# Kernel tuning notes

Hardware: AMD Instinct MI355X
Metric: run time of the kernel (lower is better)

Reference implementation:

```python
import jax, jax.numpy as jnp
import numpy as np

NB, T, NS, NC = 1024, 128, 12, 4
N = NS + NC  # stacked state+control dim


def setup_inputs() -> dict:
    key = jax.random.key(0)
    ks = jax.random.split(key, 7)
    x_init = jax.random.normal(ks[0], (NB, NS), jnp.float32)
    current_x = jax.random.normal(ks[1], (NB, T, NS), jnp.float32)
    current_u = jax.random.normal(ks[2], (NB, T, NC), jnp.float32)
    # symmetric positive-definite cost Hessian per (batch, t)
    G = 0.1 * jax.random.normal(ks[3], (NB, T, N, N), jnp.float32)
    Q = 0.5 * (G + jnp.swapaxes(G, -1, -2)) + jnp.eye(N, dtype=jnp.float32)
    p = jax.random.normal(ks[4], (NB, T, N), jnp.float32)
    # stable per-step dynamics linearizations
    A = 0.95 * jnp.eye(NS, dtype=jnp.float32) + 0.02 * jax.random.normal(ks[5], (NB, T, NS, NS), jnp.float32)
    Bmat = 0.1 * jax.random.normal(ks[6], (NB, T, NS, NC), jnp.float32)
    time = jnp.arange(T, dtype=jnp.int32)
    return {"x_init": x_init, "current_x": current_x, "current_u": current_u,
            "Q": Q, "p": p, "A": A, "Bmat": Bmat, "time": time}


def _lqr_backward(Q, p, A, Bmat):
    # time-major for scan: (T, NB, ...)
    Qs = jnp.moveaxis(Q, 1, 0)
    ps = jnp.moveaxis(p, 1, 0)
    As = jnp.moveaxis(A, 1, 0)
    Bs = jnp.moveaxis(Bmat, 1, 0)
    nb = Q.shape[0]
    V0 = jnp.zeros((nb, NS, NS), Q.dtype)  # V=0 reproduces the t==T-1 branch
    v0 = jnp.zeros((nb, NS), Q.dtype)

    def step(carry, inp):
        V, v = carry
        Qt0, pt, At, Bt = inp
        F = jnp.concatenate([At, Bt], axis=-1)          # (nb, ns, n)
        FT = jnp.swapaxes(F, -1, -2)                    # (nb, n, ns)
        Qt = Qt0 + FT @ V @ F                           # (nb, n, n)
        qt = pt + jnp.einsum('bsn,bs->bn', F, v)        # F^T v
        Qxx, Qxu = Qt[..., :NS, :NS], Qt[..., :NS, NS:]
        Qux, Quu = Qt[..., NS:, :NS], Qt[..., NS:, NS:]
        qx, qu = qt[..., :NS], qt[..., NS:]
        Quu_inv = jnp.linalg.pinv(Quu)                  # (nb, nc, nc)
        Kt = -(Quu_inv @ Qux)                           # (nb, nc, ns)
        kt = -jnp.einsum('bij,bj->bi', Quu_inv, qu)     # (nb, nc)
        KtT = jnp.swapaxes(Kt, -1, -2)
        Vn = Qxx + Qxu @ Kt + KtT @ Qux + KtT @ Quu @ Kt
        vn = (qx + jnp.einsum('bij,bj->bi', Qxu, kt)
              + jnp.einsum('bij,bj->bi', KtT, qu)
              + jnp.einsum('bij,bj->bi', KtT @ Quu, kt))
        return (Vn, vn), (Kt, kt)

    _, (K, k) = jax.lax.scan(step, (V0, v0), (Qs, ps, As, Bs), reverse=True)
    return jnp.moveaxis(K, 0, 1), jnp.moveaxis(k, 0, 1)


def _lqr_forward(x_init, current_u, Q, p, A, Bmat, K, k):
    Ks = jnp.moveaxis(K, 1, 0)
    ks_ = jnp.moveaxis(k, 1, 0)
    As = jnp.moveaxis(A, 1, 0)
    Bs = jnp.moveaxis(Bmat, 1, 0)
    cus = jnp.moveaxis(current_u, 1, 0)
    Qs = jnp.moveaxis(Q, 1, 0)
    ps = jnp.moveaxis(p, 1, 0)
    nb = x_init.shape[0]
    cost0 = jnp.zeros((nb,), x_init.dtype)

    def step(carry, inp):
        xt, cost = carry
        Kt, kt, At, Bt, cut, Qt, pt = inp
        # NOTE: original module never updates delta_x (stays zero), so delta_u == k_t
        ut = cut + kt
        xut = jnp.concatenate([xt, ut], axis=-1)        # (nb, n)
        xnext = jnp.einsum('bij,bj->bi', At, xt) + jnp.einsum('bij,bj->bi', Bt, ut)
        cost = cost + 0.5 * jnp.einsum('bi,bij,bj->b', xut, Qt, xut) + jnp.sum(xut * pt, axis=-1)
        return (xnext, cost), (xt, ut)

    (_, cost), (xs, us) = jax.lax.scan(step, (x_init, cost0), (Ks, ks_, As, Bs, cus, Qs, ps))
    # xs holds x_0..x_{T-1}, matching return of x[..., 0:-1, :]
    return jnp.moveaxis(xs, 0, 1), jnp.moveaxis(us, 0, 1), cost


def reference(x_init, current_x, current_u, Q, p, A, Bmat, time):
    K, k = _lqr_backward(Q, p, A, Bmat)
    return _lqr_forward(x_init, current_u, Q, p, A, Bmat, K, k)
```

## Files before the change

### kernel.cpp

```cpp
#include <hip/hip_runtime.h>


#define NBQ 1024
#define TT  128

__device__ __forceinline__ float dotf4(float4 a, float4 b) {
  return a.x*b.x + a.y*b.y + a.z*b.z + a.w*b.w;
}
__device__ __forceinline__ float dpp_qx1(float x) {
  return __int_as_float(__builtin_amdgcn_mov_dpp(__float_as_int(x), 0xB1, 0xF, 0xF, true));
}
__device__ __forceinline__ float dpp_qx2(float x) {
  return __int_as_float(__builtin_amdgcn_mov_dpp(__float_as_int(x), 0x4E, 0xF, 0xF, true));
}

#define BW_BODY(T_, QV, PV, CV, APrev, BPrev, ASelf, BSelf)                    \
{                                                                              \
  const int  t_   = (T_);                                                      \
  const long bt_  = b*TT + t_;                                                 \
  const int  tL_  = (t_ >= 4) ? (t_ - 4) : 0;                                  \
  const long btL_ = b*TT + tL_;                                                \
  float4 qN_ = *(const float4*)(Qg  + btL_*256 + 4*l);                         \
  float4 aN_ = *(const float4*)(Ag  + btL_*144 + aoff);                        \
  float4 bN_ = *(const float4*)(Bg  + btL_*48  + boff);                        \
  float  pN_ = pg[btL_*16 + j];                                                \
  float  cN_ = cug[btL_*4 + q4];                                               \
  float* FTc_ = (t_ & 1) ? FT1 : FT0;                                          \
  float* FTn_ = (t_ & 1) ? FT0 : FT1;                                          \
                         \
  if (l < 36) { FTn_[fta[0]]=APrev.x; FTn_[fta[1]]=APrev.y;                    \
                FTn_[fta[2]]=APrev.z; FTn_[fta[3]]=APrev.w; }                  \
  else if (l < 48) { const int kk_=l-36;                                       \
    FTn_[144+kk_]=BPrev.x; FTn_[156+kk_]=BPrev.y;                              \
    FTn_[168+kk_]=BPrev.z; FTn_[180+kk_]=BPrev.w; }                            \
                                                    \
  const float4* fj4_ = (const float4*)(FTc_ + j*12);                           \
  float4 f0_=fj4_[0], f1_=fj4_[1], f2_=fj4_[2];                                \
  const float4* gi4_ = (const float4*)(FTc_ + i4*12);                          \
  float4 g0_=gi4_[0], g1_=gi4_[1], g2_=gi4_[2];                                \
  const float4* vv4_ = (const float4*)vvS;                                     \
  float4 w0_=vv4_[0], w1_=vv4_[1], w2_=vv4_[2];                                \
  const float4* vr0_ = (const float4*)(Vs + (3*r+0)*12);                       \
  const float4* vr1_ = (const float4*)(Vs + (3*r+1)*12);                       \
  const float4* vr2_ = (const float4*)(Vs + (3*r+2)*12);                       \
  float4 va0_=vr0_[0], va1_=vr0_[1], va2_=vr0_[2];                             \
  float4 vb0_=vr1_[0], vb1_=vr1_[1], vb2_=vr1_[2];                             \
  float4 vc0_=vr2_[0], vc1_=vr2_[1], vc2_=vr2_[2];                             \
  float m0_ = dotf4(va0_,f0_) + dotf4(va1_,f1_) + dotf4(va2_,f2_);             \
  float m1_ = dotf4(vb0_,f0_) + dotf4(vb1_,f1_) + dotf4(vb2_,f2_);             \
  float m2_ = dotf4(vc0_,f0_) + dotf4(vc1_,f1_) + dotf4(vc2_,f2_);             \
  msh[(3*r+0)*16 + j] = m0_;                                                   \
  msh[(3*r+1)*16 + j] = m1_;                                                   \
  msh[(3*r+2)*16 + j] = m2_;                                                   \
  float qtv_ = PV + dotf4(w0_,f0_) + dotf4(w1_,f1_) + dotf4(w2_,f2_);          \
  float gk_[12] = {g0_.x,g0_.y,g0_.z,g0_.w, g1_.x,g1_.y,g1_.z,g1_.w,           \
                   g2_.x,g2_.y,g2_.z,g2_.w};                                   \
  float4 qt4_ = QV;                                                            \
  _Pragma("unroll")                                                            \
  for (int k2_ = 0; k2_ < 12; ++k2_) {                                         \
    float4 mk_ = *(const float4*)(msh + k2_*16 + c0);                          \
    qt4_.x += gk_[k2_]*mk_.x; qt4_.y += gk_[k2_]*mk_.y;                        \
    qt4_.z += gk_[k2_]*mk_.z; qt4_.w += gk_[k2_]*mk_.w;                        \
  }                                                                            \
  if (l >= 48)            *(float4*)(UxS + (i4-12)*16 + c0) = qt4_;            \
  if (q4 == 3 && i4 < 12) *(float4*)(XuS + i4*4) = qt4_;                       \
  if (l >= 12 && l < 16)  quS[l-12] = qtv_;                                    \
  float mm_[16];                                                               \
  _Pragma("unroll")                                                            \
  for (int c_ = 0; c_ < 4; ++c_) {                                             \
    float4 qq_ = *(const float4*)(UxS + c_*16 + 12);                           \
    mm_[c_*4+0]=qq_.x; mm_[c_*4+1]=qq_.y; mm_[c_*4+2]=qq_.z; mm_[c_*4+3]=qq_.w;\
  }                                                                            \
  float4 quv_ = *(const float4*)quS;                                           \
  float4 ux0_ = *(const float4*)(UxS + 0*16 + c0);                             \
  float4 ux1_ = *(const float4*)(UxS + 1*16 + c0);                             \
  float4 ux2_ = *(const float4*)(UxS + 2*16 + c0);                             \
  float4 ux3_ = *(const float4*)(UxS + 3*16 + c0);                             \
  float4 xr_ = *(const float4*)(XuS + min(i4,11)*4);                           \
  float4 xj_ = *(const float4*)(XuS + min(j,11)*4);                            \
                                       \
  float rdp_ = 1.0f/(mm_[0]*mm_[5] - mm_[1]*mm_[1]);                           \
  float pi00_ = mm_[5]*rdp_, pi01_ = -mm_[1]*rdp_, pi11_ = mm_[0]*rdp_;        \
  float w00_ = pi00_*mm_[2] + pi01_*mm_[6];                                    \
  float w01_ = pi00_*mm_[3] + pi01_*mm_[7];                                    \
  float w10_ = pi01_*mm_[2] + pi11_*mm_[6];                                    \
  float w11_ = pi01_*mm_[3] + pi11_*mm_[7];                                    \
  float t00_ = mm_[10] - (mm_[2]*w00_ + mm_[6]*w10_);                          \
  float t01_ = mm_[11] - (mm_[2]*w01_ + mm_[6]*w11_);                          \
  float t11_ = mm_[15] - (mm_[3]*w01_ + mm_[7]*w11_);                          \
  float rdt_ = 1.0f/(t00_*t11_ - t01_*t01_);                                   \
  float ti00_ = t11_*rdt_, ti01_ = -t01_*rdt_, ti11_ = t00_*rdt_;              \
  float u00_ = -(w00_*ti00_ + w01_*ti01_);                                     \
  float u01_ = -(w00_*ti01_ + w01_*ti11_);                                     \
  float u10_ = -(w10_*ti00_ + w11_*ti01_);                                     \
  float u11_ = -(w10_*ti01_ + w11_*ti11_);                                     \
  float i00_ = pi00_ - (u00_*w00_ + u01_*w01_);                                \
  float i01_ = pi01_ - (u00_*w10_ + u01_*w11_);                                \
  float i11_ = pi11_ - (u10_*w10_ + u11_*w11_);                                \
  float inv_[16] = { i00_, i01_, u00_, u01_,                                   \
                     i01_, i11_, u10_, u11_,                                   \
                     u00_, u10_, ti00_, ti01_,                                 \
                     u01_, u11_, ti01_, ti11_ };                               \
  float kt0_ = -(inv_[0] *quv_.x + inv_[1] *quv_.y + inv_[2] *quv_.z + inv_[3] *quv_.w); \
  float kt1_ = -(inv_[4] *quv_.x + inv_[5] *quv_.y + inv_[6] *quv_.z + inv_[7] *quv_.w); \
  float kt2_ = -(inv_[8] *quv_.x + inv_[9] *quv_.y + inv_[10]*quv_.z + inv_[11]*quv_.w); \
  float kt3_ = -(inv_[12]*quv_.x + inv_[13]*quv_.y + inv_[14]*quv_.z + inv_[15]*quv_.w); \
  float4 kc_[4];                                                               \
  _Pragma("unroll")                                                            \
  for (int c_ = 0; c_ < 4; ++c_) {                                             \
    kc_[c_].x = -(inv_[c_*4+0]*ux0_.x + inv_[c_*4+1]*ux1_.x + inv_[c_*4+2]*ux2_.x + inv_[c_*4+3]*ux3_.x); \
    kc_[c_].y = -(inv_[c_*4+0]*ux0_.y + inv_[c_*4+1]*ux1_.y + inv_[c_*4+2]*ux2_.y + inv_[c_*4+3]*ux3_.y); \
    kc_[c_].z = -(inv_[c_*4+0]*ux0_.z + inv_[c_*4+1]*ux1_.z + inv_[c_*4+2]*ux2_.z + inv_[c_*4+3]*ux3_.z); \
    kc_[c_].w = -(inv_[c_*4+0]*ux0_.w + inv_[c_*4+1]*ux1_.w + inv_[c_*4+2]*ux2_.w + inv_[c_*4+3]*ux3_.w); \
  }                                                                            \
  if (i4 < 12) {                                                               \
    float4 vn4_;                                                               \
    vn4_.x = qt4_.x + xr_.x*kc_[0].x + xr_.y*kc_[1].x + xr_.z*kc_[2].x + xr_.w*kc_[3].x; \
    vn4_.y = qt4_.y + xr_.x*kc_[0].y + xr_.y*kc_[1].y + xr_.z*kc_[2].y + xr_.w*kc_[3].y; \
    vn4_.z = qt4_.z + xr_.x*kc_[0].z + xr_.y*kc_[1].z + xr_.z*kc_[2].z + xr_.w*kc_[3].z; \
    vn4_.w = qt4_.w + xr_.x*kc_[0].w + xr_.y*kc_[1].w + xr_.z*kc_[2].w + xr_.w*kc_[3].w; \
    if (q4 < 3) *(float4*)(Vs + i4*12 + c0) = vn4_;                            \
  }                                                                            \
  if (l < 12)                                                                  \
    vvS[l] = qtv_ + xj_.x*kt0_ + xj_.y*kt1_ + xj_.z*kt2_ + xj_.w*kt3_;         \
  float uv_ = CV + ((q4==0)?kt0_:(q4==1)?kt1_:(q4==2)?kt2_:kt3_);              \
  if (l < 4) { us_out[bt_*4 + l] = uv_; uL[t_*4 + l] = uv_; }                  \
  QV = qN_; ASelf = aN_; BSelf = bN_; PV = pN_; CV = cN_;                      \
}

__global__ __launch_bounds__(64, 1) void lqr_fused(
    const float* __restrict__ Qg, const float* __restrict__ pg,
    const float* __restrict__ Ag, const float* __restrict__ Bg,
    const float* __restrict__ cug, const float* __restrict__ xinit,
    float* __restrict__ out)
{
  __shared__ __align__(16) float lds[1376];
  float* FT0 = lds;
  float* FT1 = lds + 192;
  float* Vs  = lds + 384;
  float* vvS = lds + 528;
  float* msh = lds + 544;
  float* UxS = lds + 736;
  float* XuS = lds + 800;
  float* quS = lds + 848;
  float* uL  = lds + 864;

  const int l  = threadIdx.x;
  const int j  = l & 15;
  const int r  = l >> 4;
  const int i4 = l >> 2;
  const int q4 = l & 3;
  const int c0 = q4 << 2;
  const long b = blockIdx.x;

  float* xs_out = out;
  float* us_out = out + (long)NBQ*TT*12;
  float* c_out  = out + (long)NBQ*TT*12 + (long)NBQ*TT*4;

  if (i4 < 12 && q4 < 3) *(float4*)(Vs + i4*12 + c0) = make_float4(0.f,0.f,0.f,0.f);
  if (l < 12) vvS[l] = 0.f;

  const int aoff = 4*min(l,35);
  const int boff = 4*min(max(l-36,0),11);
  int fta[4];
  #pragma unroll
  for (int e=0;e<4;++e){ int flat=4*l+e; int k=(flat*171)>>11; int n=flat-12*k; fta[e]=n*12+k; }

  const long base = b*TT;
  float4 q3v,a3v,b3v, q2v,a2v,b2v, q1v,a1v,b1v, q0v,a0v,b0v;
  float  p3v,c3v, p2v,c2v, p1v,c1v, p0v,c0vv;
  {
    long bt;
    bt = base+127; q3v=*(const float4*)(Qg+bt*256+4*l); a3v=*(const float4*)(Ag+bt*144+aoff);
                   b3v=*(const float4*)(Bg+bt*48+boff); p3v=pg[bt*16+j]; c3v=cug[bt*4+q4];
    bt = base+126; q2v=*(const float4*)(Qg+bt*256+4*l); a2v=*(const float4*)(Ag+bt*144+aoff);
                   b2v=*(const float4*)(Bg+bt*48+boff); p2v=pg[bt*16+j]; c2v=cug[bt*4+q4];
    bt = base+125; q1v=*(const float4*)(Qg+bt*256+4*l); a1v=*(const float4*)(Ag+bt*144+aoff);
                   b1v=*(const float4*)(Bg+bt*48+boff); p1v=pg[bt*16+j]; c1v=cug[bt*4+q4];
    bt = base+124; q0v=*(const float4*)(Qg+bt*256+4*l); a0v=*(const float4*)(Ag+bt*144+aoff);
                   b0v=*(const float4*)(Bg+bt*48+boff); p0v=pg[bt*16+j]; c0vv=cug[bt*4+q4];
  }
  if (l < 36) {
    FT1[fta[0]]=a3v.x; FT1[fta[1]]=a3v.y; FT1[fta[2]]=a3v.z; FT1[fta[3]]=a3v.w;
  } else if (l < 48) {
    const int kk=l-36;
    FT1[144+kk]=b3v.x; FT1[156+kk]=b3v.y; FT1[168+kk]=b3v.z; FT1[180+kk]=b3v.w;
  }

  #pragma unroll 1
  for (int tb = TT-1; tb >= 3; tb -= 4) {
    BW_BODY(tb,   q3v, p3v, c3v,  a2v, b2v,  a3v, b3v)
    BW_BODY(tb-1, q2v, p2v, c2v,  a1v, b1v,  a2v, b2v)
    BW_BODY(tb-2, q1v, p1v, c1v,  a0v, b0v,  a1v, b1v)
    BW_BODY(tb-3, q0v, p0v, c0vv, a3v, b3v,  a0v, b0v)
  }

  const int i4c = min(i4, 11);
  const int sl0 = (c0+0)<<2, sl1 = (c0+1)<<2, sl2 = (c0+2)<<2, sl3 = (c0+3)<<2;
  float s = xinit[b*12 + i4c];
  float cacc = 0.f;

  const long bt0 = base;
  float4 qfA = *(const float4*)(Qg + bt0*256 + 4*l);
  float4 ffA = (q4 < 3) ? *(const float4*)(Ag + bt0*144 + i4c*12 + c0)
                        : *(const float4*)(Bg + bt0*48  + i4c*4);
  float  pfA = pg[bt0*16 + i4];
  float4 qfB = *(const float4*)(Qg + (bt0+1)*256 + 4*l);
  float4 ffB = (q4 < 3) ? *(const float4*)(Ag + (bt0+1)*144 + i4c*12 + c0)
                        : *(const float4*)(Bg + (bt0+1)*48  + i4c*4);
  float  pfB = pg[(bt0+1)*16 + i4];
  float4 qfC = *(const float4*)(Qg + (bt0+2)*256 + 4*l);
  float4 ffC = (q4 < 3) ? *(const float4*)(Ag + (bt0+2)*144 + i4c*12 + c0)
                        : *(const float4*)(Bg + (bt0+2)*48  + i4c*4);
  float  pfC = pg[(bt0+2)*16 + i4];

  #pragma unroll 1
  for (int t = 0; t < TT; ++t) {
    const long btp = bt0 + min(t+3, TT-1);
    float4 qfD = *(const float4*)(Qg + btp*256 + 4*l);
    float4 ffD = (q4 < 3) ? *(const float4*)(Ag + btp*144 + i4c*12 + c0)
                          : *(const float4*)(Bg + btp*48  + i4c*4);
    float  pfD = pg[btp*16 + i4];

    float4 u4 = *(const float4*)(uL + t*4);

    float4 xg;
    xg.x = __shfl(s, sl0, 64); xg.y = __shfl(s, sl1, 64);
    xg.z = __shfl(s, sl2, 64); xg.w = __shfl(s, sl3, 64);
    float4 xuq = (q4 < 3) ? xg : u4;
    float xui = (i4 < 12) ? s
              : (i4 == 12) ? u4.x : (i4 == 13) ? u4.y : (i4 == 14) ? u4.z : u4.w;

    if (q4 == 0 && i4 < 12) xs_out[(bt0+t)*12 + i4] = s;

    cacc += 0.5f * xui * dotf4(qfA, xuq);
    if (q4 == 0) cacc += xui * pfA;

    float zx = dotf4(ffA, xuq);
    zx += dpp_qx1(zx);
    zx += dpp_qx2(zx);
    s = zx;

    qfA = qfB; ffA = ffB; pfA = pfB;
    qfB = qfC; ffB = ffC; pfB = pfC;
    qfC = qfD; ffC = ffD; pfC = pfD;
  }

  cacc += __shfl_xor(cacc, 32, 64);
  cacc += __shfl_xor(cacc, 16, 64);
  cacc += __shfl_xor(cacc, 8, 64);
  cacc += __shfl_xor(cacc, 4, 64);
  cacc += dpp_qx2(cacc);
  cacc += dpp_qx1(cacc);
  if (l == 0) c_out[b] = cacc;
}

extern "C" void kernel_launch(void* const* d_in, const int* in_sizes, int n_in,
                              void* d_out, int out_size, void* d_ws, size_t ws_size,
                              hipStream_t stream) {
  const float* xinit = (const float*)d_in[0];
  const float* cu = (const float*)d_in[2];
  const float* Q  = (const float*)d_in[3];
  const float* p  = (const float*)d_in[4];
  const float* A  = (const float*)d_in[5];
  const float* Bm = (const float*)d_in[6];
  float* out = (float*)d_out;

  lqr_fused<<<dim3(NBQ), dim3(64), 0, stream>>>(Q, p, A, Bm, cu, xinit, out);
}
```

Baseline: 398.2 us.

## Remap backward-pass lanes and use DPP broadcasts instead of redundant LDS reads

Reassigns the thread-to-element mapping in the backward Riccati step so each lane reads only a slice of V, the value vector, M and Quu/Qux from shared memory, then spreads the rest across the quad with DPP quad_perm broadcasts. The A/B global loads are restructured into scalar strided loads with a new transpose-store pattern into the F^T buffer, and the Qt row is taken from the lane's own F values. The goal is less LDS traffic and fewer bank conflicts on the serial per-timestep critical path. In exchange it adds DPP instructions and non-vectorized global loads, and it makes the index mapping more complex.

Measured after the change: 383.1 us. 1.04x faster.

```diff
diff --git a/kernel.cpp b/kernel.cpp
--- a/kernel.cpp
+++ b/kernel.cpp
@@ -13,71 +13,82 @@
 __device__ __forceinline__ float dpp_qx2(float x) {
   return __int_as_float(__builtin_amdgcn_mov_dpp(__float_as_int(x), 0x4E, 0xF, 0xF, true));
 }
-
-#define BW_BODY(T_, QV, PV, CV, APrev, BPrev, ASelf, BSelf)                    \
+template<int Q> __device__ __forceinline__ float4 bcast4(float4 v) {
+  float4 r;
+  r.x = __int_as_float(__builtin_amdgcn_mov_dpp(__float_as_int(v.x), Q*0x55, 0xF, 0xF, true));
+  r.y = __int_as_float(__builtin_amdgcn_mov_dpp(__float_as_int(v.y), Q*0x55, 0xF, 0xF, true));
+  r.z = __int_as_float(__builtin_amdgcn_mov_dpp(__float_as_int(v.z), Q*0x55, 0xF, 0xF, true));
+  r.w = __int_as_float(__builtin_amdgcn_mov_dpp(__float_as_int(v.w), Q*0x55, 0xF, 0xF, true));
+  return r;
+}
+
+#define MKS(K, O, MY)  { float4 mk_ = bcast4<O>(MY);                           \
+  qt4_.x += gk_[K]*mk_.x; qt4_.y += gk_[K]*mk_.y;                              \
+  qt4_.z += gk_[K]*mk_.z; qt4_.w += gk_[K]*mk_.w; }
+
+#define BW_BODY(T_, QV, PV, CV, P0,P1,P2,P3, S0,S1,S2,S3)                      \
 {                                                                              \
   const int  t_   = (T_);                                                      \
   const long bt_  = b*TT + t_;                                                 \
-  const int  tL_  = (t_ >= 4) ? (t_ - 4) : 0;                                  \
-  const long btL_ = b*TT + tL_;                                                \
-  float4 qN_ = *(const float4*)(Qg  + btL_*256 + 4*l);                         \
-  float4 aN_ = *(const float4*)(Ag  + btL_*144 + aoff);                        \
-  float4 bN_ = *(const float4*)(Bg  + btL_*48  + boff);                        \
+  const long btL_ = b*TT + ((t_ >= 4) ? (t_ - 4) : 0);                         \
+  float4 qN_ = *(const float4*)(Qg + btL_*256 + qoff);                         \
+  const float* fpL_ = lt48 ? (Ag + btL_*144 + l) : (Bg + btL_*48 + bm_);       \
+  float fN0_ = fpL_[0], fN1_ = fpL_[fstr_], fN2_ = fpL_[2*fstr_], fN3_ = fpL_[foff3];  \
   float  pN_ = pg[btL_*16 + j];                                                \
   float  cN_ = cug[btL_*4 + q4];                                               \
   float* FTc_ = (t_ & 1) ? FT1 : FT0;                                          \
   float* FTn_ = (t_ & 1) ? FT0 : FT1;                                          \
-                         \
-  if (l < 36) { FTn_[fta[0]]=APrev.x; FTn_[fta[1]]=APrev.y;                    \
-                FTn_[fta[2]]=APrev.z; FTn_[fta[3]]=APrev.w; }                  \
-  else if (l < 48) { const int kk_=l-36;                                       \
-    FTn_[144+kk_]=BPrev.x; FTn_[156+kk_]=BPrev.y;                              \
-    FTn_[168+kk_]=BPrev.z; FTn_[180+kk_]=BPrev.w; }                            \
-                                                    \
+                     \
+  if (lt48)      { FTn_[ba] = P0; FTn_[ba+4] = P1; FTn_[ba+8] = P2; }          \
+  else if (lt60) { FTn_[bb] = P0; FTn_[bb+3] = P1; FTn_[bb+6] = P2; FTn_[bb+9] = P3; } \
+   \
   const float4* fj4_ = (const float4*)(FTc_ + j*12);                           \
   float4 f0_=fj4_[0], f1_=fj4_[1], f2_=fj4_[2];                                \
-  const float4* gi4_ = (const float4*)(FTc_ + i4*12);                          \
-  float4 g0_=gi4_[0], g1_=gi4_[1], g2_=gi4_[2];                                \
-  const float4* vv4_ = (const float4*)vvS;                                     \
-  float4 w0_=vv4_[0], w1_=vv4_[1], w2_=vv4_[2];                                \
-  const float4* vr0_ = (const float4*)(Vs + (3*r+0)*12);                       \
-  const float4* vr1_ = (const float4*)(Vs + (3*r+1)*12);                       \
-  const float4* vr2_ = (const float4*)(Vs + (3*r+2)*12);                       \
-  float4 va0_=vr0_[0], va1_=vr0_[1], va2_=vr0_[2];                             \
-  float4 vb0_=vr1_[0], vb1_=vr1_[1], vb2_=vr1_[2];                             \
-  float4 vc0_=vr2_[0], vc1_=vr2_[1], vc2_=vr2_[2];                             \
-  float m0_ = dotf4(va0_,f0_) + dotf4(va1_,f1_) + dotf4(va2_,f2_);             \
-  float m1_ = dotf4(vb0_,f0_) + dotf4(vb1_,f1_) + dotf4(vb2_,f2_);             \
-  float m2_ = dotf4(vc0_,f0_) + dotf4(vc1_,f1_) + dotf4(vc2_,f2_);             \
+  const float4* vrow_ = (const float4*)(Vs + (3*r + dmin)*12);                 \
+  float4 mv0_=vrow_[0], mv1_=vrow_[1], mv2_=vrow_[2];                          \
+  float4 mw_ = *(const float4*)(vvS + 4*dmin);                                 \
+                                      \
+  float m0_, m1_, m2_;                                                         \
+  { float4 r0_=bcast4<0>(mv0_), r1_=bcast4<0>(mv1_), r2_=bcast4<0>(mv2_);      \
+    m0_ = dotf4(r0_,f0_)+dotf4(r1_,f1_)+dotf4(r2_,f2_); }                      \
+  { float4 r0_=bcast4<1>(mv0_), r1_=bcast4<1>(mv1_), r2_=bcast4<1>(mv2_);      \
+    m1_ = dotf4(r0_,f0_)+dotf4(r1_,f1_)+dotf4(r2_,f2_); }                      \
+  { float4 r0_=bcast4<2>(mv0_), r1_=bcast4<2>(mv1_), r2_=bcast4<2>(mv2_);      \
+    m2_ = dotf4(r0_,f0_)+dotf4(r1_,f1_)+dotf4(r2_,f2_); }                      \
   msh[(3*r+0)*16 + j] = m0_;                                                   \
   msh[(3*r+1)*16 + j] = m1_;                                                   \
   msh[(3*r+2)*16 + j] = m2_;                                                   \
-  float qtv_ = PV + dotf4(w0_,f0_) + dotf4(w1_,f1_) + dotf4(w2_,f2_);          \
-  float gk_[12] = {g0_.x,g0_.y,g0_.z,g0_.w, g1_.x,g1_.y,g1_.z,g1_.w,           \
-                   g2_.x,g2_.y,g2_.z,g2_.w};                                   \
+                \
+  float qtv_;                                                                  \
+  { float4 w0_=bcast4<0>(mw_), w1_=bcast4<1>(mw_), w2_=bcast4<2>(mw_);         \
+    qtv_ = PV + dotf4(w0_,f0_)+dotf4(w1_,f1_)+dotf4(w2_,f2_); }                \
+                    \
+  float gk_[12] = {f0_.x,f0_.y,f0_.z,f0_.w, f1_.x,f1_.y,f1_.z,f1_.w,           \
+                   f2_.x,f2_.y,f2_.z,f2_.w};                                   \
+  float4 mys0_ = *(const float4*)(msh + (3*q4+0)*16 + cb4);                    \
+  float4 mys1_ = *(const float4*)(msh + (3*q4+1)*16 + cb4);                    \
+  float4 mys2_ = *(const float4*)(msh + (3*q4+2)*16 + cb4);                    \
   float4 qt4_ = QV;                                                            \
-  _Pragma("unroll")                                                            \
-  for (int k2_ = 0; k2_ < 12; ++k2_) {                                         \
-    float4 mk_ = *(const float4*)(msh + k2_*16 + c0);                          \
-    qt4_.x += gk_[k2_]*mk_.x; qt4_.y += gk_[k2_]*mk_.y;                        \
-    qt4_.z += gk_[k2_]*mk_.z; qt4_.w += gk_[k2_]*mk_.w;                        \
-  }                                                                            \
-  if (l >= 48)            *(float4*)(UxS + (i4-12)*16 + c0) = qt4_;            \
-  if (q4 == 3 && i4 < 12) *(float4*)(XuS + i4*4) = qt4_;                       \
-  if (l >= 12 && l < 16)  quS[l-12] = qtv_;                                    \
+  MKS(0,0,mys0_) MKS(1,0,mys1_) MKS(2,0,mys2_)                                 \
+  MKS(3,1,mys0_) MKS(4,1,mys1_) MKS(5,1,mys2_)                                 \
+  MKS(6,2,mys0_) MKS(7,2,mys1_) MKS(8,2,mys2_)                                 \
+  MKS(9,3,mys0_) MKS(10,3,mys1_) MKS(11,3,mys2_)                               \
+                                            \
+  if (j >= 12)           *(float4*)(UxS + (j-12)*16 + cb4) = qt4_;             \
+  if (cb == 3 && j < 12) *(float4*)(XuS + j*4) = qt4_;                         \
+  if (l >= 12 && l < 16) quS[l-12] = qtv_;                                     \
+                                         \
+  float4 myquu_ = *(const float4*)(UxS + q4*16 + 12);                          \
+  float4 myux_  = *(const float4*)(UxS + q4*16 + cb4);                         \
+  float4 quv_   = *(const float4*)quS;                                         \
+  float4 xr_    = *(const float4*)(XuS + jc*4);                                \
   float mm_[16];                                                               \
-  _Pragma("unroll")                                                            \
-  for (int c_ = 0; c_ < 4; ++c_) {                                             \
-    float4 qq_ = *(const float4*)(UxS + c_*16 + 12);                           \
-    mm_[c_*4+0]=qq_.x; mm_[c_*4+1]=qq_.y; mm_[c_*4+2]=qq_.z; mm_[c_*4+3]=qq_.w;\
-  }                                                                            \
-  float4 quv_ = *(const float4*)quS;                                           \
-  float4 ux0_ = *(const float4*)(UxS + 0*16 + c0);                             \
-  float4 ux1_ = *(const float4*)(UxS + 1*16 + c0);                             \
-  float4 ux2_ = *(const float4*)(UxS + 2*16 + c0);                             \
-  float4 ux3_ = *(const float4*)(UxS + 3*16 + c0);                             \
-  float4 xr_ = *(const float4*)(XuS + min(i4,11)*4);                           \
-  float4 xj_ = *(const float4*)(XuS + min(j,11)*4);                            \
+  { float4 t0_=bcast4<0>(myquu_); mm_[0]=t0_.x; mm_[1]=t0_.y; mm_[2]=t0_.z; mm_[3]=t0_.w; \
+    float4 t1_=bcast4<1>(myquu_); mm_[4]=t1_.x; mm_[5]=t1_.y; mm_[6]=t1_.z; mm_[7]=t1_.w; \
+    float4 t2_=bcast4<2>(myquu_); mm_[8]=t2_.x; mm_[9]=t2_.y; mm_[10]=t2_.z; mm_[11]=t2_.w; \
+    float4 t3_=bcast4<3>(myquu_); mm_[12]=t3_.x; mm_[13]=t3_.y; mm_[14]=t3_.z; mm_[15]=t3_.w; } \
+  float4 ux0_=bcast4<0>(myux_), ux1_=bcast4<1>(myux_),                         \
+         ux2_=bcast4<2>(myux_), ux3_=bcast4<3>(myux_);                         \
                                        \
   float rdp_ = 1.0f/(mm_[0]*mm_[5] - mm_[1]*mm_[1]);                           \
   float pi00_ = mm_[5]*rdp_, pi01_ = -mm_[1]*rdp_, pi11_ = mm_[0]*rdp_;        \
@@ -113,19 +124,19 @@
     kc_[c_].z = -(inv_[c_*4+0]*ux0_.z + inv_[c_*4+1]*ux1_.z + inv_[c_*4+2]*ux2_.z + inv_[c_*4+3]*ux3_.z); \
     kc_[c_].w = -(inv_[c_*4+0]*ux0_.w + inv_[c_*4+1]*ux1_.w + inv_[c_*4+2]*ux2_.w + inv_[c_*4+3]*ux3_.w); \
   }                                                                            \
-  if (i4 < 12) {                                                               \
+  if (j < 12) {                                                                \
     float4 vn4_;                                                               \
     vn4_.x = qt4_.x + xr_.x*kc_[0].x + xr_.y*kc_[1].x + xr_.z*kc_[2].x + xr_.w*kc_[3].x; \
     vn4_.y = qt4_.y + xr_.x*kc_[0].y + xr_.y*kc_[1].y + xr_.z*kc_[2].y + xr_.w*kc_[3].y; \
     vn4_.z = qt4_.z + xr_.x*kc_[0].z + xr_.y*kc_[1].z + xr_.z*kc_[2].z + xr_.w*kc_[3].z; \
     vn4_.w = qt4_.w + xr_.x*kc_[0].w + xr_.y*kc_[1].w + xr_.z*kc_[2].w + xr_.w*kc_[3].w; \
-    if (q4 < 3) *(float4*)(Vs + i4*12 + c0) = vn4_;                            \
+    if (cb < 3) *(float4*)(Vs + j*12 + cb4) = vn4_;                            \
   }                                                                            \
   if (l < 12)                                                                  \
-    vvS[l] = qtv_ + xj_.x*kt0_ + xj_.y*kt1_ + xj_.z*kt2_ + xj_.w*kt3_;         \
+    vvS[l] = qtv_ + xr_.x*kt0_ + xr_.y*kt1_ + xr_.z*kt2_ + xr_.w*kt3_;         \
   float uv_ = CV + ((q4==0)?kt0_:(q4==1)?kt1_:(q4==2)?kt2_:kt3_);              \
   if (l < 4) { us_out[bt_*4 + l] = uv_; uL[t_*4 + l] = uv_; }                  \
-  QV = qN_; ASelf = aN_; BSelf = bN_; PV = pN_; CV = cN_;                      \
+  QV = qN_; S0 = fN0_; S1 = fN1_; S2 = fN2_; S3 = fN3_; PV = pN_; CV = cN_;    \
 }
 
 __global__ __launch_bounds__(64, 1) void lqr_fused(
@@ -145,80 +156,87 @@
   float* quS = lds + 848;
   float* uL  = lds + 864;
 
-  const int l  = threadIdx.x;
-  const int j  = l & 15;
-  const int r  = l >> 4;
-  const int i4 = l >> 2;
-  const int q4 = l & 3;
-  const int c0 = q4 << 2;
-  const long b = blockIdx.x;
+  const int l    = threadIdx.x;
+  const int j    = l & 15;
+  const int r    = l >> 4;
+  const int q4   = l & 3;
+  const int cb   = l >> 4;
+  const int cb4  = cb << 2;
+  const int dmin = (q4 < 2) ? q4 : 2;
+  const int jc   = (j < 12) ? j : 11;
+  const long b   = blockIdx.x;
+  const bool lt48 = (l < 48);
+  const bool lt60 = (l < 60);
+  const int  bm_  = lt48 ? 0 : ((l - 48) % 12);
+  const int  fstr_ = lt48 ? 48 : 12;
+  const int  foff3 = lt48 ? 96 : 36;
+  const int  ba = (l % 12) * 12 + l / 12;
+  const int  bb = 144 + ((l - 48) & 3) * 12 + ((l - 48) >> 2);
+  const int  qoff = j * 16 + cb4;
 
   float* xs_out = out;
   float* us_out = out + (long)NBQ*TT*12;
   float* c_out  = out + (long)NBQ*TT*12 + (long)NBQ*TT*4;
 
-  if (i4 < 12 && q4 < 3) *(float4*)(Vs + i4*12 + c0) = make_float4(0.f,0.f,0.f,0.f);
+  if (j < 12 && cb < 3) *(float4*)(Vs + j*12 + cb4) = make_float4(0.f,0.f,0.f,0.f);
   if (l < 12) vvS[l] = 0.f;
 
-  const int aoff = 4*min(l,35);
-  const int boff = 4*min(max(l-36,0),11);
-  int fta[4];
-  #pragma unroll
-  for (int e=0;e<4;++e){ int flat=4*l+e; int k=(flat*171)>>11; int n=flat-12*k; fta[e]=n*12+k; }
-
   const long base = b*TT;
-  float4 q3v,a3v,b3v, q2v,a2v,b2v, q1v,a1v,b1v, q0v,a0v,b0v;
-  float  p3v,c3v, p2v,c2v, p1v,c1v, p0v,c0vv;
+  float4 q3v,q2v,q1v,q0v;
+  float  p3v,c3v,p2v,c2v,p1v,c1v,p0v,c0v;
+  float  f3a,f3b,f3c,f3d, f2a,f2b,f2c,f2d, f1a,f1b,f1c,f1d, f0a,f0b,f0c,f0d;
   {
     long bt;
-    bt = base+127; q3v=*(const float4*)(Qg+bt*256+4*l); a3v=*(const float4*)(Ag+bt*144+aoff);
-                   b3v=*(const float4*)(Bg+bt*48+boff); p3v=pg[bt*16+j]; c3v=cug[bt*4+q4];
-    bt = base+126; q2v=*(const float4*)(Qg+bt*256+4*l); a2v=*(const float4*)(Ag+bt*144+aoff);
-                   b2v=*(const float4*)(Bg+bt*48+boff); p2v=pg[bt*16+j]; c2v=cug[bt*4+q4];
-    bt = base+125; q1v=*(const float4*)(Qg+bt*256+4*l); a1v=*(const float4*)(Ag+bt*144+aoff);
-                   b1v=*(const float4*)(Bg+bt*48+boff); p1v=pg[bt*16+j]; c1v=cug[bt*4+q4];
-    bt = base+124; q0v=*(const float4*)(Qg+bt*256+4*l); a0v=*(const float4*)(Ag+bt*144+aoff);
-                   b0v=*(const float4*)(Bg+bt*48+boff); p0v=pg[bt*16+j]; c0vv=cug[bt*4+q4];
+    bt = base+127; q3v=*(const float4*)(Qg+bt*256+qoff); p3v=pg[bt*16+j]; c3v=cug[bt*4+q4];
+    { const float* fp = lt48 ? (Ag+bt*144+l) : (Bg+bt*48+bm_);
+      f3a=fp[0]; f3b=fp[fstr_]; f3c=fp[2*fstr_]; f3d=fp[foff3]; }
+    bt = base+126; q2v=*(const float4*)(Qg+bt*256+qoff); p2v=pg[bt*16+j]; c2v=cug[bt*4+q4];
+    { const float* fp = lt48 ? (Ag+bt*144+l) : (Bg+bt*48+bm_);
+      f2a=fp[0]; f2b=fp[fstr_]; f2c=fp[2*fstr_]; f2d=fp[foff3]; }
+    bt = base+125; q1v=*(const float4*)(Qg+bt*256+qoff); p1v=pg[bt*16+j]; c1v=cug[bt*4+q4];
+    { const float* fp = lt48 ? (Ag+bt*144+l) : (Bg+bt*48+bm_);
+      f1a=fp[0]; f1b=fp[fstr_]; f1c=fp[2*fstr_]; f1d=fp[foff3]; }
+    bt = base+124; q0v=*(const float4*)(Qg+bt*256+qoff); p0v=pg[bt*16+j]; c0v=cug[bt*4+q4];
+    { const float* fp = lt48 ? (Ag+bt*144+l) : (Bg+bt*48+bm_);
+      f0a=fp[0]; f0b=fp[fstr_]; f0c=fp[2*fstr_]; f0d=fp[foff3]; }
   }
-  if (l < 36) {
-    FT1[fta[0]]=a3v.x; FT1[fta[1]]=a3v.y; FT1[fta[2]]=a3v.z; FT1[fta[3]]=a3v.w;
-  } else if (l < 48) {
-    const int kk=l-36;
-    FT1[144+kk]=b3v.x; FT1[156+kk]=b3v.y; FT1[168+kk]=b3v.z; FT1[180+kk]=b3v.w;
-  }
+  if (lt48)      { FT1[ba] = f3a; FT1[ba+4] = f3b; FT1[ba+8] = f3c; }
+  else if (lt60) { FT1[bb] = f3a; FT1[bb+3] = f3b; FT1[bb+6] = f3c; FT1[bb+9] = f3d; }
 
   #pragma unroll 1
   for (int tb = TT-1; tb >= 3; tb -= 4) {
-    BW_BODY(tb,   q3v, p3v, c3v,  a2v, b2v,  a3v, b3v)
-    BW_BODY(tb-1, q2v, p2v, c2v,  a1v, b1v,  a2v, b2v)
-    BW_BODY(tb-2, q1v, p1v, c1v,  a0v, b0v,  a1v, b1v)
-    BW_BODY(tb-3, q0v, p0v, c0vv, a3v, b3v,  a0v, b0v)
+    BW_BODY(tb,   q3v, p3v, c3v,  f2a,f2b,f2c,f2d,  f3a,f3b,f3c,f3d)
+    BW_BODY(tb-1, q2v, p2v, c2v,  f1a,f1b,f1c,f1d,  f2a,f2b,f2c,f2d)
+    BW_BODY(tb-2, q1v, p1v, c1v,  f0a,f0b,f0c,f0d,  f1a,f1b,f1c,f1d)
+    BW_BODY(tb-3, q0v, p0v, c0v,  f3a,f3b,f3c,f3d,  f0a,f0b,f0c,f0d)
   }
 
-  const int i4c = min(i4, 11);
-  const int sl0 = (c0+0)<<2, sl1 = (c0+1)<<2, sl2 = (c0+2)<<2, sl3 = (c0+3)<<2;
+  const int i4  = l >> 2;
+  const int c0f = q4 << 2;
+  const int i4c = (i4 < 12) ? i4 : 11;
+  const int sl0 = (c0f+0)<<2, sl1 = (c0f+1)<<2, sl2 = (c0f+2)<<2, sl3 = (c0f+3)<<2;
   float s = xinit[b*12 + i4c];
   float cacc = 0.f;
 
   const long bt0 = base;
   float4 qfA = *(const float4*)(Qg + bt0*256 + 4*l);
-  float4 ffA = (q4 < 3) ? *(const float4*)(Ag + bt0*144 + i4c*12 + c0)
+  float4 ffA = (q4 < 3) ? *(const float4*)(Ag + bt0*144 + i4c*12 + c0f)
                         : *(const float4*)(Bg + bt0*48  + i4c*4);
   float  pfA = pg[bt0*16 + i4];
   float4 qfB = *(const float4*)(Qg + (bt0+1)*256 + 4*l);
-  float4 ffB = (q4 < 3) ? *(const float4*)(Ag + (bt0+1)*144 + i4c*12 + c0)
+  float4 ffB = (q4 < 3) ? *(const float4*)(Ag + (bt0+1)*144 + i4c*12 + c0f)
                         : *(const float4*)(Bg + (bt0+1)*48  + i4c*4);
   float  pfB = pg[(bt0+1)*16 + i4];
   float4 qfC = *(const float4*)(Qg + (bt0+2)*256 + 4*l);
-  float4 ffC = (q4 < 3) ? *(const float4*)(Ag + (bt0+2)*144 + i4c*12 + c0)
+  float4 ffC = (q4 < 3) ? *(const float4*)(Ag + (bt0+2)*144 + i4c*12 + c0f)
                         : *(const float4*)(Bg + (bt0+2)*48  + i4c*4);
   float  pfC = pg[(bt0+2)*16 + i4];
 
   #pragma unroll 1
   for (int t = 0; t < TT; ++t) {
-    const long btp = bt0 + min(t+3, TT-1);
+    const long btp = bt0 + ((t+3 < TT-1) ? t+3 : TT-1);
     float4 qfD = *(const float4*)(Qg + btp*256 + 4*l);
-    float4 ffD = (q4 < 3) ? *(const float4*)(Ag + btp*144 + i4c*12 + c0)
+    float4 ffD = (q4 < 3) ? *(const float4*)(Ag + btp*144 + i4c*12 + c0f)
                           : *(const float4*)(Bg + btp*48  + i4c*4);
     float  pfD = pg[btp*16 + i4];
 
```
